# Kernel optimization log

Hardware: AMD Instinct MI355X
Metric: run time of the kernel (lower is better)

## Reference

```python
import jax, jax.numpy as jnp
import numpy as np

# module hyperparameters (init kwargs)
D_MODEL = 1024
NUM_HEADS = 16
D_K = D_MODEL // NUM_HEADS
WINDOW_SIZE = 256
GLOBAL_TOKENS = 64
SEQ_LEN = 4096
BATCH = 1
NEG_INF = float('-inf')


def build_local_window_mask(seq_len, window_size, global_tokens):
    # 0 where attention is allowed, -inf where blocked
    i = jnp.arange(seq_len)[:, None]
    j = jnp.arange(seq_len)[None, :]
    allowed = (i < global_tokens) | (j < global_tokens) | (jnp.abs(i - j) <= window_size)
    return jnp.where(allowed, 0.0, NEG_INF).astype(jnp.float32)


def setup_inputs() -> dict:
    key = jax.random.key(0)
    ks = jax.random.split(key, 12)
    s = 1.0 / np.sqrt(D_MODEL)
    inp = {
        'q': jax.random.normal(ks[0], (BATCH, SEQ_LEN, D_MODEL), jnp.float32),
        'k': jax.random.normal(ks[1], (BATCH, SEQ_LEN, D_MODEL), jnp.float32),
        'v': jax.random.normal(ks[2], (BATCH, SEQ_LEN, D_MODEL), jnp.float32),
        # nn.Linear weights: shape (out, in), applied as x @ W.T + b
        'w_q': jax.random.normal(ks[3], (D_MODEL, D_MODEL), jnp.float32) * s,
        'b_q': jax.random.normal(ks[4], (D_MODEL,), jnp.float32) * s,
        'w_k': jax.random.normal(ks[5], (D_MODEL, D_MODEL), jnp.float32) * s,
        'b_k': jax.random.normal(ks[6], (D_MODEL,), jnp.float32) * s,
        'w_v': jax.random.normal(ks[7], (D_MODEL, D_MODEL), jnp.float32) * s,
        'b_v': jax.random.normal(ks[8], (D_MODEL,), jnp.float32) * s,
        'w_o': jax.random.normal(ks[9], (D_MODEL, D_MODEL), jnp.float32) * s,
        'b_o': jax.random.normal(ks[10], (D_MODEL,), jnp.float32) * s,
    }
    return inp


def reference(q, k, v, w_q, b_q, w_k, b_k, w_v, b_v, w_o, b_o):
    B, S, _ = q.shape
    scale = 1.0 / np.sqrt(D_K)

    def proj(x, w, b):  # (B,S,D) -> (B,H,S,Dk)
        y = x @ w.T + b
        return y.reshape(B, S, NUM_HEADS, D_K).transpose(0, 2, 1, 3)

    Q = proj(q, w_q, b_q)
    K = proj(k, w_k, b_k)
    V = proj(v, w_v, b_v)

    local_mask = build_local_window_mask(S, WINDOW_SIZE, GLOBAL_TOKENS)  # (S,S)
    scores = jnp.einsum('bhqd,bhkd->bhqk', Q, K) * scale + local_mask[None, None]
    attn = jax.nn.softmax(scores, axis=-1)
    out = jnp.einsum('bhqk,bhkd->bhqd', attn, V)  # (B,H,S,Dk)
    out = out.transpose(0, 2, 1, 3).reshape(B, S, D_MODEL)
    return out @ w_o.T + b_o
```

## Files before the change

kernel.cpp:

```cpp
#include <hip/hip_runtime.h>

#define S_LEN 4096
#define DMODEL 1024
#define NHEADS 16
#define DKH 64
#define WIN 256
#define GTOK 64
#define NSPLIT 8

typedef unsigned short u16t;
typedef __attribute__((ext_vector_type(8))) short short8;
typedef __attribute__((ext_vector_type(4))) float f32x4;

__device__ __forceinline__ u16t f2bf(float x) {
  union { float f; unsigned int u; } v; v.f = x;
  unsigned int r = v.u + 0x7FFFu + ((v.u >> 16) & 1u);
  return (u16t)(r >> 16);
}

__device__ __forceinline__ unsigned int cvtpk(float lo, float hi) {
  unsigned int r;
  asm("v_cvt_pk_bf16_f32 %0, %1, %2" : "=v"(r) : "v"(lo), "v"(hi));
  return r;
}

__device__ __forceinline__ void gload_lds16(const u16t* g, u16t* l) {
  __builtin_amdgcn_global_load_lds(
      (const __attribute__((address_space(1))) void*)g,
      (__attribute__((address_space(3))) void*)l, 16, 0, 0);
}

__global__ void cvt_all(const float* __restrict__ s0, const float* __restrict__ s1,
                        const float* __restrict__ s2, const float* __restrict__ s3,
                        const float* __restrict__ s4, const float* __restrict__ s5,
                        const float* __restrict__ s6,
                        u16t* __restrict__ d0, u16t* __restrict__ d1,
                        u16t* __restrict__ d2, u16t* __restrict__ d3,
                        u16t* __restrict__ d4, u16t* __restrict__ d5,
                        u16t* __restrict__ d6) {
  size_t i = (size_t)blockIdx.x * 1024 + threadIdx.x * 4;
  const float* s; u16t* d; size_t local;
  if (i < ((size_t)4 << 20)) {
    int which = (int)(i >> 20);
    local = i & ((1u << 20) - 1);
    s = which == 0 ? s0 : which == 1 ? s1 : which == 2 ? s2 : s3;
    d = which == 0 ? d0 : which == 1 ? d1 : which == 2 ? d2 : d3;
  } else {
    size_t j = i - ((size_t)4 << 20);
    int which = (int)(j >> 22);
    local = j & ((1u << 22) - 1);
    s = which == 0 ? s4 : which == 1 ? s5 : s6;
    d = which == 0 ? d4 : which == 1 ? d5 : d6;
  }
  float4 f = *(const float4*)(s + local);
  unsigned int lo = (unsigned int)f2bf(f.x) | ((unsigned int)f2bf(f.y) << 16);
  unsigned int hi = (unsigned int)f2bf(f.z) | ((unsigned int)f2bf(f.w) << 16);
  *(uint2*)(d + local) = make_uint2(lo, hi);
}

#define BN 128
#define GBK 64

template<int OUT_F32, int BMT, int BIAS_ROW>
__device__ __forceinline__
void gemm_body(u16t* __restrict__ smem,
               const u16t* __restrict__ A, const u16t* __restrict__ B,
               const float* __restrict__ bias, void* __restrict__ Y,
               int N, int K, float alpha, int m0, int n0)
{
  constexpr int MF = BMT / 32;
  constexpr int CA_ISS = BMT * 2 / 64;
  constexpr int TILE = (BMT + BN) * GBK;

  const int tid = threadIdx.x;
  const int lane = tid & 63;
  const int lr = lane & 15, lg = lane >> 4;
  const int w = tid >> 6;
  const int wm = (w >> 1) * (MF * 16), wn = (w & 1) * 64;

  f32x4 acc[MF][4] = {};
  const int nk = K / GBK;

  auto stage = [&](int buf, int kt) {
    u16t* sA = smem + buf * TILE;
    u16t* sB = sA + BMT * GBK;
#pragma unroll
    for (int i = 0; i < CA_ISS; ++i) {
      int c0 = w * (BMT * 2) + i * 64;
      int c = c0 + lane;
      int row = c >> 3, g = (c & 7) ^ (row & 7);
      gload_lds16(A + (size_t)(m0 + row) * K + kt * GBK + g * 8, sA + (size_t)c0 * 8);
    }
#pragma unroll
    for (int i = 0; i < 4; ++i) {
      int c0 = w * 256 + i * 64;
      int c = c0 + lane;
      int row = c >> 3, g = (c & 7) ^ (row & 7);
      gload_lds16(B + (size_t)(n0 + row) * K + kt * GBK + g * 8, sB + (size_t)c0 * 8);
    }
  };

  stage(0, 0);
  __syncthreads();

  for (int kt = 0; kt < nk; ++kt) {
    const int buf = kt & 1;
    if (kt + 1 < nk) stage(buf ^ 1, kt + 1);

    const u16t* sA = smem + buf * TILE;
    const u16t* sB = sA + BMT * GBK;

    short8 af[MF][2], bf[4][2];
#pragma unroll
    for (int mf = 0; mf < MF; ++mf)
#pragma unroll
      for (int kk = 0; kk < 2; ++kk) {
        int s = ((kk * 4 + lg) ^ (lr & 7));
        af[mf][kk] = *(const short8*)&sA[(wm + mf * 16 + lr) * GBK + s * 8];
      }
#pragma unroll
    for (int nf = 0; nf < 4; ++nf)
#pragma unroll
      for (int kk = 0; kk < 2; ++kk) {
        int s = ((kk * 4 + lg) ^ (lr & 7));
        bf[nf][kk] = *(const short8*)&sB[(wn + nf * 16 + lr) * GBK + s * 8];
      }
    __builtin_amdgcn_s_setprio(1);
#pragma unroll
    for (int kk = 0; kk < 2; ++kk)
#pragma unroll
      for (int mf = 0; mf < MF; ++mf)
#pragma unroll
        for (int nf = 0; nf < 4; ++nf)
          acc[mf][nf] = __builtin_amdgcn_mfma_f32_16x16x32_bf16(af[mf][kk], bf[nf][kk], acc[mf][nf], 0, 0, 0);
    __builtin_amdgcn_s_setprio(0);

    if (kt + 1 < nk) __syncthreads();
  }

#pragma unroll
  for (int nf = 0; nf < 4; ++nf) {
    int col = n0 + wn + nf * 16 + lr;
    float bvc = BIAS_ROW ? 0.f : bias[col];
#pragma unroll
    for (int mf = 0; mf < MF; ++mf)
#pragma unroll
      for (int r = 0; r < 4; ++r) {
        int row = m0 + wm + mf * 16 + lg * 4 + r;
        float bv = BIAS_ROW ? bias[row] : bvc;
        float v = (acc[mf][nf][r] + bv) * alpha;
        if (OUT_F32) ((float*)Y)[(size_t)row * N + col] = v;
        else         ((u16t*)Y)[(size_t)row * N + col] = f2bf(v);
      }
  }
}

#define QSCALE 0.18033688011112042f
__global__ __launch_bounds__(256)
void gemm_qkv(const u16t* __restrict__ xq, const u16t* __restrict__ xk, const u16t* __restrict__ xv,
              const u16t* __restrict__ wq, const u16t* __restrict__ wk, const u16t* __restrict__ wv,
              const float* __restrict__ bq, const float* __restrict__ bk, const float* __restrict__ bv,
              u16t* __restrict__ Qp, u16t* __restrict__ Kp, u16t* __restrict__ Vt)
{
  __shared__ __align__(16) u16t smem[2 * (128 + 128) * GBK];

  int b = blockIdx.x;
  int wid = (b & 7) * 96 + (b >> 3);
  int z = wid >> 8;
  int rem = wid & 255;
  if (z == 0) {
    gemm_body<0, 128, 0>(smem, xq, wq, bq, Qp, DMODEL, DMODEL, QSCALE, (rem >> 3) * 128, (rem & 7) * BN);
  } else if (z == 1) {
    gemm_body<0, 128, 0>(smem, xk, wk, bk, Kp, DMODEL, DMODEL, 1.0f, (rem >> 3) * 128, (rem & 7) * BN);
  } else {
    gemm_body<0, 128, 1>(smem, wv, xv, bv, Vt, S_LEN, DMODEL, 1.0f, (rem & 7) * 128, (rem >> 3) * BN);
  }
}

__global__ __launch_bounds__(256)
void gemm_o(const u16t* __restrict__ A, const u16t* __restrict__ B,
            const float* __restrict__ bias, float* __restrict__ Y)
{
  __shared__ __align__(16) u16t smem[2 * (64 + 128) * GBK];

  int b = blockIdx.x;
  int wid = (b & 7) * 64 + (b >> 3);
  int my = wid >> 3, mx = wid & 7;
  gemm_body<1, 64, 0>(smem, A, B, bias, Y, DMODEL, DMODEL, 1.0f, my * 64, mx * BN);
}

__global__ __launch_bounds__(256)
void attn_kernel(const u16t* __restrict__ Qp, const u16t* __restrict__ Kp,
                 const u16t* __restrict__ Vt, u16t* __restrict__ AO,
                 float* __restrict__ pacc, float* __restrict__ pml)
{
  __shared__ __align__(16) u16t sK[2][64 * 64];
  __shared__ __align__(16) u16t sV[2][64 * 64];
  __shared__ __align__(16) u16t sP[4][16 * 64];

  const int b = blockIdx.x;
  const int wid = (b & 7) * 142 + (b >> 3);
  const int h = wid / 71;
  const int x = wid % 71;

  const int tid = threadIdx.x, w = tid >> 6, lane = tid & 63;
  const int lr = lane & 15, lg = lane >> 4;

  const bool windowed = (x < 63);
  const int qb = windowed ? (x + 1) : 0;
  const int split = windowed ? 0 : (x - 63);
  const int qw = qb * 64 + w * 16;

  short8 qf[2];
#pragma unroll
  for (int kk = 0; kk < 2; ++kk)
    qf[kk] = *(const short8*)(Qp + (size_t)(qw + lr) * DMODEL + h * DKH + kk * 32 + lg * 8);

  f32x4 acc[4] = {};
  float m_run = -1e30f;
  float l_run = 0.f;

  int lo = 1, nkv;
  if (windowed) {
    lo = (qb - 4 < 1) ? 1 : qb - 4;
    int hi = (qb + 4 > 63) ? 63 : qb + 4;
    nkv = hi - lo + 2;
  } else {
    nkv = 64 / NSPLIT;
  }

#define KVB(idx) (windowed ? ((idx) == 0 ? 0 : lo + (idx) - 1) : (split * (64 / NSPLIT) + (idx)))

  auto stage = [&](int buf, int kvb) {
    int kv0 = kvb * 64;
#pragma unroll
    for (int j = 0; j < 2; ++j) {
      int c = tid + j * 256;
      int row = c >> 3, g = (c & 7) ^ (row & 7);
      gload_lds16(Kp + (size_t)(kv0 + row) * DMODEL + h * DKH + g * 8, &sK[buf][c * 8]);
    }
#pragma unroll
    for (int j = 0; j < 2; ++j) {
      int c = tid + j * 256;
      int row = c >> 3, g = (c & 7) ^ (row & 7);
      gload_lds16(Vt + (size_t)(h * DKH + row) * S_LEN + kv0 + g * 8, &sV[buf][c * 8]);
    }
  };

  stage(0, KVB(0));
  __syncthreads();

  for (int idx = 0; idx < nkv; ++idx) {
    const int buf = idx & 1;
    const int kvb = KVB(idx);
    const int kv0 = kvb * 64;

    if (idx + 1 < nkv) stage(buf ^ 1, KVB(idx + 1));

    f32x4 sacc[4] = {};
    __builtin_amdgcn_s_setprio(1);
#pragma unroll
    for (int kk = 0; kk < 2; ++kk)
#pragma unroll
      for (int nf = 0; nf < 4; ++nf) {
        int s = ((kk * 4 + lg) ^ (lr & 7));
        short8 kf = *(const short8*)&sK[buf][(nf * 16 + lr) * 64 + s * 8];
        sacc[nf] = __builtin_amdgcn_mfma_f32_16x16x32_bf16(kf, qf[kk], sacc[nf], 0, 0, 0);
      }
    __builtin_amdgcn_s_setprio(0);

    if (windowed && (kvb == qb + 4 || (kvb == qb - 4 && kvb > 0))) {
      int qg = qw + lr;
#pragma unroll
      for (int nf = 0; nf < 4; ++nf)
#pragma unroll
        for (int r = 0; r < 4; ++r) {
          int sg = kv0 + nf * 16 + lg * 4 + r;
          int diff = qg - sg; if (diff < 0) diff = -diff;
          if (diff > WIN) sacc[nf][r] = -1e30f;
        }
    }

    float rm0 = fmaxf(fmaxf(sacc[0][0], sacc[0][1]), sacc[0][2]);
    float rm1 = fmaxf(fmaxf(sacc[0][3], sacc[1][0]), sacc[1][1]);
    float rm2 = fmaxf(fmaxf(sacc[1][2], sacc[1][3]), sacc[2][0]);
    float rm3 = fmaxf(fmaxf(sacc[2][1], sacc[2][2]), sacc[2][3]);
    float rm4 = fmaxf(fmaxf(sacc[3][0], sacc[3][1]), sacc[3][2]);
    float rm = fmaxf(fmaxf(rm0, rm1), fmaxf(fmaxf(rm2, rm3), fmaxf(rm4, sacc[3][3])));

    if (!__all(rm <= m_run + 11.0f)) {
      rm = fmaxf(rm, __shfl_xor(rm, 16));
      rm = fmaxf(rm, __shfl_xor(rm, 32));
      float mnew = fmaxf(m_run, rm);
      float corr = exp2f(m_run - mnew);
      m_run = mnew;
      l_run *= corr;
      float cq[4];
#pragma unroll
      for (int r = 0; r < 4; ++r) cq[r] = __shfl(corr, lg * 4 + r);
#pragma unroll
      for (int nf = 0; nf < 4; ++nf)
#pragma unroll
        for (int r = 0; r < 4; ++r) acc[nf][r] *= cq[r];
    }

    float p[4][4];
    float rs = 0.f;
#pragma unroll
    for (int nf = 0; nf < 4; ++nf)
#pragma unroll
      for (int r = 0; r < 4; ++r) {
        float e = exp2f(sacc[nf][r] - m_run);
        p[nf][r] = e;
        rs += e;
      }
    l_run += rs;

#pragma unroll
    for (int nf = 0; nf < 4; ++nf) {
      unsigned int lo32 = cvtpk(p[nf][0], p[nf][1]);
      unsigned int hi32 = cvtpk(p[nf][2], p[nf][3]);
      int blk = (nf * 2 + (lg >> 1)) ^ (lr & 7);
      *(uint2*)&sP[w][lr * 64 + blk * 8 + (lg & 1) * 4] = make_uint2(lo32, hi32);
    }

#pragma unroll
    for (int kk = 0; kk < 2; ++kk) {
      short8 pf = *(const short8*)&sP[w][lr * 64 + (((kk * 4 + lg) ^ (lr & 7))) * 8];
      __builtin_amdgcn_s_setprio(1);
#pragma unroll
      for (int nf = 0; nf < 4; ++nf) {
        int s = ((kk * 4 + lg) ^ (lr & 7));
        short8 vf = *(const short8*)&sV[buf][(nf * 16 + lr) * 64 + s * 8];
        acc[nf] = __builtin_amdgcn_mfma_f32_16x16x32_bf16(pf, vf, acc[nf], 0, 0, 0);
      }
      __builtin_amdgcn_s_setprio(0);
    }

    if (idx + 1 < nkv) __syncthreads();
  }
#undef KVB

  l_run += __shfl_xor(l_run, 16);
  l_run += __shfl_xor(l_run, 32);

  if (windowed) {
    float lq[4];
#pragma unroll
    for (int r = 0; r < 4; ++r) lq[r] = __shfl(l_run, lg * 4 + r);
#pragma unroll
    for (int nf = 0; nf < 4; ++nf)
#pragma unroll
      for (int r = 0; r < 4; ++r) {
        float v = acc[nf][r] / lq[r];
        AO[(size_t)(qw + lg * 4 + r) * DMODEL + h * DKH + nf * 16 + lr] = f2bf(v);
      }
  } else {
    const int pbase = (h * NSPLIT + split) * 64;
#pragma unroll
    for (int nf = 0; nf < 4; ++nf)
#pragma unroll
      for (int r = 0; r < 4; ++r)
        pacc[(size_t)(pbase + w * 16 + lg * 4 + r) * 64 + nf * 16 + lr] = acc[nf][r];
    if (lane < 16) {
      int bb = (pbase + w * 16 + lane) * 2;
      pml[bb] = m_run;
      pml[bb + 1] = l_run;
    }
  }
}

__global__ __launch_bounds__(256)
void merge_kernel(const float* __restrict__ pacc, const float* __restrict__ pml,
                  u16t* __restrict__ AO)
{
  const int h = blockIdx.x;
  const int tid = threadIdx.x;
  const int row = tid >> 2;
  const int d0 = (tid & 3) * 16;

  float M = -1e30f;
#pragma unroll
  for (int s = 0; s < NSPLIT; ++s)
    M = fmaxf(M, pml[((h * NSPLIT + s) * 64 + row) * 2]);

  float L = 0.f;
  float o[16];
#pragma unroll
  for (int e = 0; e < 16; ++e) o[e] = 0.f;

#pragma unroll
  for (int s = 0; s < NSPLIT; ++s) {
    int b = ((h * NSPLIT + s) * 64 + row) * 2;
    float sc = exp2f(pml[b] - M);
    L += pml[b + 1] * sc;
    const float4* a = (const float4*)(pacc + ((size_t)(h * NSPLIT + s) * 64 + row) * 64 + d0);
#pragma unroll
    for (int q4 = 0; q4 < 4; ++q4) {
      float4 av = a[q4];
      o[q4 * 4 + 0] += av.x * sc;
      o[q4 * 4 + 1] += av.y * sc;
      o[q4 * 4 + 2] += av.z * sc;
      o[q4 * 4 + 3] += av.w * sc;
    }
  }
  float inv = 1.f / L;
#pragma unroll
  for (int e = 0; e < 16; ++e)
    AO[(size_t)row * DMODEL + h * DKH + d0 + e] = f2bf(o[e] * inv);
}

extern "C" void kernel_launch(void* const* d_in, const int* in_sizes, int n_in,
                              void* d_out, int out_size, void* d_ws, size_t ws_size,
                              hipStream_t stream) {
  const float* q   = (const float*)d_in[0];
  const float* k   = (const float*)d_in[1];
  const float* v   = (const float*)d_in[2];
  const float* w_q = (const float*)d_in[3];
  const float* b_q = (const float*)d_in[4];
  const float* w_k = (const float*)d_in[5];
  const float* b_k = (const float*)d_in[6];
  const float* w_v = (const float*)d_in[7];
  const float* b_v = (const float*)d_in[8];
  const float* w_o = (const float*)d_in[9];
  const float* b_o = (const float*)d_in[10];

  u16t* ws = (u16t*)d_ws;
  const size_t SZX = (size_t)S_LEN * DMODEL;
  const size_t SZW = (size_t)DMODEL * DMODEL;
  u16t* xq  = ws;
  u16t* xk  = xq + SZX;
  u16t* xv  = xk + SZX;
  u16t* wb0 = xv + SZX;
  u16t* wb1 = wb0 + SZW;
  u16t* wb2 = wb1 + SZW;
  u16t* wb3 = wb2 + SZW;
  u16t* Qp  = wb3 + SZW;
  u16t* Kp  = Qp + SZX;
  u16t* Vt  = Kp + SZX;
  u16t* AO  = xk;
  float* pacc = (float*)xq;
  float* pml  = pacc + (size_t)NHEADS * NSPLIT * 64 * 64;

  dim3 blk(256);

  cvt_all<<<(int)((4 * SZW + 3 * SZX) / 1024), blk, 0, stream>>>(
      w_q, w_k, w_v, w_o, q, k, v, wb0, wb1, wb2, wb3, xq, xk, xv);

  gemm_qkv<<<768, blk, 0, stream>>>(xq, xk, xv, wb0, wb1, wb2, b_q, b_k, b_v, Qp, Kp, Vt);

  attn_kernel<<<(63 + NSPLIT) * NHEADS, blk, 0, stream>>>(Qp, Kp, Vt, AO, pacc, pml);
  merge_kernel<<<NHEADS, blk, 0, stream>>>(pacc, pml, AO);

  gemm_o<<<512, blk, 0, stream>>>(AO, wb3, b_o, (float*)d_out);
}
```

Measured before the change: 110.0 us.

## Process two query blocks per attention workgroup with 512 threads

The attention kernel now runs 512-thread workgroups that each cover two consecutive 64-row query blocks, so staged K/V tiles are shared by eight waves instead of four and total K/V traffic drops. The grid shrinks accordingly, and global-token splits use only four of the eight waves. The masking condition is widened to cover the wider window union, and the final block pair handles a single block with half the waves idle. The trade-off is more KV iterations per block over the union window, fewer blocks, and idle waves in the split path.

```diff
diff --git a/kernel.cpp b/kernel.cpp
--- a/kernel.cpp
+++ b/kernel.cpp
@@ -189,27 +189,31 @@
   gemm_body<1, 64, 0>(smem, A, B, bias, Y, DMODEL, DMODEL, 1.0f, my * 64, mx * BN);
 }
 
-__global__ __launch_bounds__(256)
+__global__ __launch_bounds__(512)
 void attn_kernel(const u16t* __restrict__ Qp, const u16t* __restrict__ Kp,
                  const u16t* __restrict__ Vt, u16t* __restrict__ AO,
                  float* __restrict__ pacc, float* __restrict__ pml)
 {
   __shared__ __align__(16) u16t sK[2][64 * 64];
   __shared__ __align__(16) u16t sV[2][64 * 64];
-  __shared__ __align__(16) u16t sP[4][16 * 64];
+  __shared__ __align__(16) u16t sP[8][16 * 64];
 
   const int b = blockIdx.x;
-  const int wid = (b & 7) * 142 + (b >> 3);
-  const int h = wid / 71;
-  const int x = wid % 71;
+  const int wid = (b & 7) * 80 + (b >> 3);
+  const int h = wid / 40;
+  const int x = wid % 40;
 
   const int tid = threadIdx.x, w = tid >> 6, lane = tid & 63;
   const int lr = lane & 15, lg = lane >> 4;
 
-  const bool windowed = (x < 63);
-  const int qb = windowed ? (x + 1) : 0;
-  const int split = windowed ? 0 : (x - 63);
-  const int qw = qb * 64 + w * 16;
+  const bool windowed = (x < 32);
+  const int qbl = windowed ? (2 * x + 1) : 0;
+  const int qbh = windowed ? ((x == 31) ? 63 : 2 * x + 2) : 0;
+  const int split = windowed ? 0 : (x - 32);
+
+  const bool active = windowed ? !(x == 31 && w >= 4) : (w < 4);
+  const int wq = windowed ? ((x == 31) ? (w & 3) : w) : (w & 3);
+  const int qw = qbl * 64 + wq * 16;
 
   short8 qf[2];
 #pragma unroll
@@ -222,8 +226,8 @@
 
   int lo = 1, nkv;
   if (windowed) {
-    lo = (qb - 4 < 1) ? 1 : qb - 4;
-    int hi = (qb + 4 > 63) ? 63 : qb + 4;
+    lo = (qbl - 4 < 1) ? 1 : qbl - 4;
+    int hi = (qbh + 4 > 63) ? 63 : qbh + 4;
     nkv = hi - lo + 2;
   } else {
     nkv = 64 / NSPLIT;
@@ -233,18 +237,10 @@
 
   auto stage = [&](int buf, int kvb) {
     int kv0 = kvb * 64;
-#pragma unroll
-    for (int j = 0; j < 2; ++j) {
-      int c = tid + j * 256;
-      int row = c >> 3, g = (c & 7) ^ (row & 7);
-      gload_lds16(Kp + (size_t)(kv0 + row) * DMODEL + h * DKH + g * 8, &sK[buf][c * 8]);
-    }
-#pragma unroll
-    for (int j = 0; j < 2; ++j) {
-      int c = tid + j * 256;
-      int row = c >> 3, g = (c & 7) ^ (row & 7);
-      gload_lds16(Vt + (size_t)(h * DKH + row) * S_LEN + kv0 + g * 8, &sV[buf][c * 8]);
-    }
+    int c = tid;
+    int row = c >> 3, g = (c & 7) ^ (row & 7);
+    gload_lds16(Kp + (size_t)(kv0 + row) * DMODEL + h * DKH + g * 8, &sK[buf][c * 8]);
+    gload_lds16(Vt + (size_t)(h * DKH + row) * S_LEN + kv0 + g * 8, &sV[buf][c * 8]);
   };
 
   stage(0, KVB(0));
@@ -269,7 +265,7 @@
       }
     __builtin_amdgcn_s_setprio(0);
 
-    if (windowed && (kvb == qb + 4 || (kvb == qb - 4 && kvb > 0))) {
+    if (windowed && kvb > 0 && (kvb <= qbh - 4 || kvb >= qbl + 4)) {
       int qg = qw + lr;
 #pragma unroll
       for (int nf = 0; nf < 4; ++nf)
@@ -345,25 +341,27 @@
   l_run += __shfl_xor(l_run, 32);
 
   if (windowed) {
-    float lq[4];
-#pragma unroll
-    for (int r = 0; r < 4; ++r) lq[r] = __shfl(l_run, lg * 4 + r);
+    if (active) {
+      float lq[4];
+#pragma unroll
+      for (int r = 0; r < 4; ++r) lq[r] = __shfl(l_run, lg * 4 + r);
+#pragma unroll
+      for (int nf = 0; nf < 4; ++nf)
+#pragma unroll
+        for (int r = 0; r < 4; ++r) {
+          float v = acc[nf][r] / lq[r];
+          AO[(size_t)(qw + lg * 4 + r) * DMODEL + h * DKH + nf * 16 + lr] = f2bf(v);
+        }
+    }
+  } else if (active) {
+    const int pbase = (h * NSPLIT + split) * 64;
 #pragma unroll
     for (int nf = 0; nf < 4; ++nf)
 #pragma unroll
-      for (int r = 0; r < 4; ++r) {
-        float v = acc[nf][r] / lq[r];
-        AO[(size_t)(qw + lg * 4 + r) * DMODEL + h * DKH + nf * 16 + lr] = f2bf(v);
-      }
-  } else {
-    const int pbase = (h * NSPLIT + split) * 64;
-#pragma unroll
-    for (int nf = 0; nf < 4; ++nf)
-#pragma unroll
       for (int r = 0; r < 4; ++r)
-        pacc[(size_t)(pbase + w * 16 + lg * 4 + r) * 64 + nf * 16 + lr] = acc[nf][r];
+        pacc[(size_t)(pbase + wq * 16 + lg * 4 + r) * 64 + nf * 16 + lr] = acc[nf][r];
     if (lane < 16) {
-      int bb = (pbase + w * 16 + lane) * 2;
+      int bb = (pbase + wq * 16 + lane) * 2;
       pml[bb] = m_run;
       pml[bb + 1] = l_run;
     }
@@ -449,7 +447,7 @@
 
   gemm_qkv<<<768, blk, 0, stream>>>(xq, xk, xv, wb0, wb1, wb2, b_q, b_k, b_v, Qp, Kp, Vt);
 
-  attn_kernel<<<(63 + NSPLIT) * NHEADS, blk, 0, stream>>>(Qp, Kp, Vt, AO, pacc, pml);
+  attn_kernel<<<(32 + NSPLIT) * NHEADS, dim3(512), 0, stream>>>(Qp, Kp, Vt, AO, pacc, pml);
   merge_kernel<<<NHEADS, blk, 0, stream>>>(pacc, pml, AO);
 
   gemm_o<<<512, blk, 0, stream>>>(AO, wb3, b_o, (float*)d_out);
```

After: 115.2 us. 1.05x slower.

## Use single-buffered 128-wide K tiles in QKV GEMM, templatize K depth

Applied to the files above, without the earlier changes.

The GEMM body now takes the K-tile depth and double-buffering as template parameters. The QKV projection GEMM switches to a single-buffered 128-deep K tile (same 64KB LDS) with a sync before and after each stage, halving the number of K iterations. The output GEMM keeps double-buffered 64-deep tiles. The QKV path gives up overlap of global loads with MFMA in exchange for fewer barriers and iterations, so it depends on occupancy to hide load latency.

```diff
diff --git a/kernel.cpp b/kernel.cpp
--- a/kernel.cpp
+++ b/kernel.cpp
@@ -59,9 +59,8 @@
 }
 
 #define BN 128
-#define GBK 64
-
-template<int OUT_F32, int BMT, int BIAS_ROW>
+
+template<int OUT_F32, int BMT, int BIAS_ROW, int GBKT, int DBUF>
 __device__ __forceinline__
 void gemm_body(u16t* __restrict__ smem,
                const u16t* __restrict__ A, const u16t* __restrict__ B,
@@ -69,8 +68,11 @@
                int N, int K, float alpha, int m0, int n0)
 {
   constexpr int MF = BMT / 32;
-  constexpr int CA_ISS = BMT * 2 / 64;
-  constexpr int TILE = (BMT + BN) * GBK;
+  constexpr int COL8 = GBKT / 8;
+  constexpr int KKN = GBKT / 32;
+  constexpr int IA = BMT * COL8 / 256;
+  constexpr int IB = BN * COL8 / 256;
+  constexpr int TILE = (BMT + BN) * GBKT;
 
   const int tid = threadIdx.x;
   const int lane = tid & 63;
@@ -79,63 +81,60 @@
   const int wm = (w >> 1) * (MF * 16), wn = (w & 1) * 64;
 
   f32x4 acc[MF][4] = {};
-  const int nk = K / GBK;
+  const int nk = K / GBKT;
 
   auto stage = [&](int buf, int kt) {
     u16t* sA = smem + buf * TILE;
-    u16t* sB = sA + BMT * GBK;
-#pragma unroll
-    for (int i = 0; i < CA_ISS; ++i) {
-      int c0 = w * (BMT * 2) + i * 64;
-      int c = c0 + lane;
-      int row = c >> 3, g = (c & 7) ^ (row & 7);
-      gload_lds16(A + (size_t)(m0 + row) * K + kt * GBK + g * 8, sA + (size_t)c0 * 8);
-    }
-#pragma unroll
-    for (int i = 0; i < 4; ++i) {
-      int c0 = w * 256 + i * 64;
-      int c = c0 + lane;
-      int row = c >> 3, g = (c & 7) ^ (row & 7);
-      gload_lds16(B + (size_t)(n0 + row) * K + kt * GBK + g * 8, sB + (size_t)c0 * 8);
+    u16t* sB = sA + BMT * GBKT;
+#pragma unroll
+    for (int i = 0; i < IA; ++i) {
+      int c = i * 256 + tid;
+      int row = c / COL8, g = (c % COL8) ^ (row & (COL8 - 1));
+      gload_lds16(A + (size_t)(m0 + row) * K + kt * GBKT + g * 8, sA + (size_t)c * 8);
+    }
+#pragma unroll
+    for (int i = 0; i < IB; ++i) {
+      int c = i * 256 + tid;
+      int row = c / COL8, g = (c % COL8) ^ (row & (COL8 - 1));
+      gload_lds16(B + (size_t)(n0 + row) * K + kt * GBKT + g * 8, sB + (size_t)c * 8);
     }
   };
 
-  stage(0, 0);
-  __syncthreads();
+  if (DBUF) { stage(0, 0); __syncthreads(); }
 
   for (int kt = 0; kt < nk; ++kt) {
-    const int buf = kt & 1;
-    if (kt + 1 < nk) stage(buf ^ 1, kt + 1);
+    const int buf = DBUF ? (kt & 1) : 0;
+    if (DBUF) {
+      if (kt + 1 < nk) stage(buf ^ 1, kt + 1);
+    } else {
+      if (kt) __syncthreads();
+      stage(0, kt);
+      __syncthreads();
+    }
 
     const u16t* sA = smem + buf * TILE;
-    const u16t* sB = sA + BMT * GBK;
-
-    short8 af[MF][2], bf[4][2];
-#pragma unroll
-    for (int mf = 0; mf < MF; ++mf)
-#pragma unroll
-      for (int kk = 0; kk < 2; ++kk) {
-        int s = ((kk * 4 + lg) ^ (lr & 7));
-        af[mf][kk] = *(const short8*)&sA[(wm + mf * 16 + lr) * GBK + s * 8];
-      }
-#pragma unroll
-    for (int nf = 0; nf < 4; ++nf)
-#pragma unroll
-      for (int kk = 0; kk < 2; ++kk) {
-        int s = ((kk * 4 + lg) ^ (lr & 7));
-        bf[nf][kk] = *(const short8*)&sB[(wn + nf * 16 + lr) * GBK + s * 8];
-      }
-    __builtin_amdgcn_s_setprio(1);
-#pragma unroll
-    for (int kk = 0; kk < 2; ++kk)
+    const u16t* sB = sA + BMT * GBKT;
+
+#pragma unroll
+    for (int kk = 0; kk < KKN; ++kk) {
+      short8 af2[MF], bf2[4];
+      int s = ((kk * 4 + lg) ^ (lr & (COL8 - 1)));
 #pragma unroll
       for (int mf = 0; mf < MF; ++mf)
+        af2[mf] = *(const short8*)&sA[(wm + mf * 16 + lr) * GBKT + s * 8];
+#pragma unroll
+      for (int nf = 0; nf < 4; ++nf)
+        bf2[nf] = *(const short8*)&sB[(wn + nf * 16 + lr) * GBKT + s * 8];
+      __builtin_amdgcn_s_setprio(1);
+#pragma unroll
+      for (int mf = 0; mf < MF; ++mf)
 #pragma unroll
         for (int nf = 0; nf < 4; ++nf)
-          acc[mf][nf] = __builtin_amdgcn_mfma_f32_16x16x32_bf16(af[mf][kk], bf[nf][kk], acc[mf][nf], 0, 0, 0);
-    __builtin_amdgcn_s_setprio(0);
-
-    if (kt + 1 < nk) __syncthreads();
+          acc[mf][nf] = __builtin_amdgcn_mfma_f32_16x16x32_bf16(af2[mf], bf2[nf], acc[mf][nf], 0, 0, 0);
+      __builtin_amdgcn_s_setprio(0);
+    }
+
+    if (DBUF && kt + 1 < nk) __syncthreads();
   }
 
 #pragma unroll
@@ -162,18 +161,18 @@
               const float* __restrict__ bq, const float* __restrict__ bk, const float* __restrict__ bv,
               u16t* __restrict__ Qp, u16t* __restrict__ Kp, u16t* __restrict__ Vt)
 {
-  __shared__ __align__(16) u16t smem[2 * (128 + 128) * GBK];
+  __shared__ __align__(16) u16t smem[(128 + 128) * 128];
 
   int b = blockIdx.x;
   int wid = (b & 7) * 96 + (b >> 3);
   int z = wid >> 8;
   int rem = wid & 255;
   if (z == 0) {
-    gemm_body<0, 128, 0>(smem, xq, wq, bq, Qp, DMODEL, DMODEL, QSCALE, (rem >> 3) * 128, (rem & 7) * BN);
+    gemm_body<0, 128, 0, 128, 0>(smem, xq, wq, bq, Qp, DMODEL, DMODEL, QSCALE, (rem >> 3) * 128, (rem & 7) * BN);
   } else if (z == 1) {
-    gemm_body<0, 128, 0>(smem, xk, wk, bk, Kp, DMODEL, DMODEL, 1.0f, (rem >> 3) * 128, (rem & 7) * BN);
+    gemm_body<0, 128, 0, 128, 0>(smem, xk, wk, bk, Kp, DMODEL, DMODEL, 1.0f, (rem >> 3) * 128, (rem & 7) * BN);
   } else {
-    gemm_body<0, 128, 1>(smem, wv, xv, bv, Vt, S_LEN, DMODEL, 1.0f, (rem & 7) * 128, (rem >> 3) * BN);
+    gemm_body<0, 128, 1, 128, 0>(smem, wv, xv, bv, Vt, S_LEN, DMODEL, 1.0f, (rem & 7) * 128, (rem >> 3) * BN);
   }
 }
 
@@ -181,12 +180,12 @@
 void gemm_o(const u16t* __restrict__ A, const u16t* __restrict__ B,
             const float* __restrict__ bias, float* __restrict__ Y)
 {
-  __shared__ __align__(16) u16t smem[2 * (64 + 128) * GBK];
+  __shared__ __align__(16) u16t smem[2 * (64 + 128) * 64];
 
   int b = blockIdx.x;
   int wid = (b & 7) * 64 + (b >> 3);
   int my = wid >> 3, mx = wid & 7;
-  gemm_body<1, 64, 0>(smem, A, B, bias, Y, DMODEL, DMODEL, 1.0f, my * 64, mx * BN);
+  gemm_body<1, 64, 0, 64, 1>(smem, A, B, bias, Y, DMODEL, DMODEL, 1.0f, my * 64, mx * BN);
 }
 
 __global__ __launch_bounds__(256)
```

Measured after the change: 107.1 us. 2.6% less time.
